# Performance work log

Hardware: AMD Instinct MI355X
Metric: run time of the kernel (lower is better)

## Reference

```python
import math
import jax, jax.numpy as jnp
import numpy as np

T, B, E, H = 1024, 4, 1024, 16
DH = E // H
NUM_BUCKETS = 32
MAX_DISTANCE = 128


def setup_inputs() -> dict:
    key = jax.random.key(0)
    ks = jax.random.split(key, 12)
    s = 0.02
    return {
        "query": jax.random.normal(ks[0], (T, B, E), dtype=jnp.float32),
        "q_w": jax.random.normal(ks[1], (E, E), dtype=jnp.float32) * s,
        "q_b": jax.random.normal(ks[2], (E,), dtype=jnp.float32) * s,
        "k_w": jax.random.normal(ks[3], (E, E), dtype=jnp.float32) * s,
        "k_b": jax.random.normal(ks[4], (E,), dtype=jnp.float32) * s,
        "v_w": jax.random.normal(ks[5], (E, E), dtype=jnp.float32) * s,
        "v_b": jax.random.normal(ks[6], (E,), dtype=jnp.float32) * s,
        "out_w": jax.random.normal(ks[7], (E, E), dtype=jnp.float32) * s,
        "out_b": jnp.zeros((E,), dtype=jnp.float32),
        "rel_bias": jax.random.normal(ks[8], (NUM_BUCKETS, H), dtype=jnp.float32) * s,
        "grep_w": jax.random.normal(ks[9], (8, DH), dtype=jnp.float32) * s,
        "grep_b": jax.random.normal(ks[10], (8,), dtype=jnp.float32) * s,
        "grep_a": jnp.ones((1, H, 1, 1), dtype=jnp.float32),
    }


def _relative_position_buckets(qlen, klen):
    # bidirectional T5-style bucketing
    ctx = jnp.arange(qlen, dtype=jnp.int32)[:, None]
    mem = jnp.arange(klen, dtype=jnp.int32)[None, :]
    rp = mem - ctx  # [qlen, klen]
    n = NUM_BUCKETS // 2
    buckets = (rp > 0).astype(jnp.int32) * n
    arp = jnp.abs(rp)
    max_exact = n // 2
    is_small = arp < max_exact
    # guard log(0): values at arp<max_exact are never selected from the large branch
    large = max_exact + (
        jnp.log(jnp.maximum(arp, 1).astype(jnp.float32) / max_exact)
        / math.log(MAX_DISTANCE / max_exact)
        * (n - max_exact)
    ).astype(jnp.int32)
    large = jnp.minimum(large, n - 1)
    return buckets + jnp.where(is_small, arp, large)


def reference(query, q_w, q_b, k_w, k_b, v_w, v_b, out_w, out_b, rel_bias, grep_w, grep_b, grep_a):
    tgt_len, bsz, embed_dim = query.shape
    scaling = DH ** -0.5

    # relative-position bias [H, T, T]
    buckets = _relative_position_buckets(tgt_len, tgt_len)
    pos_bias = rel_bias[buckets]                     # [T, T, H]
    pos_bias = jnp.transpose(pos_bias, (2, 0, 1))    # [H, T, T]

    # GRU-style gate computed from the *unprojected* query, per head
    qh_raw = jnp.transpose(query, (1, 0, 2)).reshape(bsz, tgt_len, H, DH)
    qh_raw = jnp.transpose(qh_raw, (0, 2, 1, 3))     # [B, H, T, DH]
    g = jnp.einsum("bhtd,ed->bhte", qh_raw, grep_w) + grep_b  # [B,H,T,8]
    g = jax.nn.sigmoid(g.reshape(bsz, H, tgt_len, 2, 4).sum(-1))  # [B,H,T,2]
    gate_a, gate_b = g[..., 0:1], g[..., 1:2]        # [B,H,T,1]
    gate_a_1 = gate_a * (gate_b * grep_a - 1.0) + 2.0
    attn_bias = gate_a_1 * pos_bias[None]            # [B, H, T, T]

    # QKV projections (self-attention: k,v from query)
    q = (query @ q_w.T + q_b) * scaling
    k = query @ k_w.T + k_b
    v = query @ v_w.T + v_b
    qh = jnp.transpose(q.reshape(tgt_len, bsz, H, DH), (1, 2, 0, 3))  # [B,H,T,DH]
    kh = jnp.transpose(k.reshape(tgt_len, bsz, H, DH), (1, 2, 0, 3))
    vh = jnp.transpose(v.reshape(tgt_len, bsz, H, DH), (1, 2, 0, 3))

    scores = jnp.einsum("bhtd,bhsd->bhts", qh, kh) + attn_bias
    probs = jax.nn.softmax(scores, axis=-1)
    ctx = jnp.einsum("bhts,bhsd->bhtd", probs, vh)   # [B,H,T,DH]
    ctx = jnp.transpose(ctx, (2, 0, 1, 3)).reshape(tgt_len, bsz, embed_dim)
    out = ctx @ out_w.T + out_b                      # [T, B, E]
    return out
```

## Files before the change

kernel.cpp:

```cpp
#include <hip/hip_runtime.h>
#include <math.h>

#define T_ 1024
#define B_ 4
#define E_ 1024
#define H_ 16
#define DH_ 64

#define LOG2E 1.44269504088896f

typedef __attribute__((ext_vector_type(8))) __bf16 bf16x8;
typedef __attribute__((ext_vector_type(4))) __bf16 bf16x4;
typedef __attribute__((ext_vector_type(4))) float f32x4;

__device__ __forceinline__ __bf16 f2bf(float x){
  union { unsigned short u; __bf16 b; } cv;
  unsigned u32 = __float_as_uint(x);
  cv.u = (unsigned short)((u32 + 0x7fffu + ((u32 >> 16) & 1u)) >> 16);
  return cv.b;
}
__device__ __forceinline__ __bf16 f2bf_fast(float x){
  union { unsigned short u; __bf16 b; } cv;
  cv.u = (unsigned short)((__float_as_uint(x) + 0x8000u) >> 16);
  return cv.b;
}

__device__ __forceinline__ void glds16(const void* g, void* l){
  __builtin_amdgcn_global_load_lds(
      (__attribute__((address_space(1))) void*)(void*)g,
      (__attribute__((address_space(3))) void*)l,
      16, 0, 0);
}

__global__ __launch_bounds__(256) void prep_kernel(
    const float* __restrict__ q_w, const float* __restrict__ k_w,
    const float* __restrict__ v_w, const float* __restrict__ out_w,
    __bf16* __restrict__ wq, __bf16* __restrict__ wk,
    __bf16* __restrict__ wv, __bf16* __restrict__ wo,
    const float* __restrict__ query, const float* __restrict__ gw,
    const float* __restrict__ gb, const float* __restrict__ ga,
    float* __restrict__ gates, __bf16* __restrict__ qbf,
    const float* __restrict__ rel_bias, float* __restrict__ tab)
{
  const int bid = blockIdx.x;
  const int tid = threadIdx.x;
  if (bid < 4096){
    const float* a; __bf16* o;
    switch (bid >> 10){
      case 0: a = q_w;  o = wq; break;
      case 1: a = k_w;  o = wk; break;
      case 2: a = v_w;  o = wv; break;
      default: a = out_w; o = wo; break;
    }
    int i = ((bid & 1023) * 256 + tid) * 4;
    float4 v = *(const float4*)(a + i);
    bf16x4 r;
    r[0] = f2bf(v.x); r[1] = f2bf(v.y); r[2] = f2bf(v.z); r[3] = f2bf(v.w);
    *(bf16x4*)(o + i) = r;
  } else if (bid < 4352){
    int t = (bid - 4096) * 4 + (tid >> 6);
    int bh = tid & 63;
    int h = bh & 15;
    const float* q = query + (size_t)t * E_ * B_ + bh * 64;
    __bf16* qo = qbf + (size_t)t * E_ * B_ + bh * 64;
    float g[8];
    #pragma unroll
    for (int e = 0; e < 8; e++) g[e] = gb[e];
    #pragma unroll
    for (int c = 0; c < 8; c++){
      float4 v0 = *(const float4*)(q + c * 8);
      float4 v1 = *(const float4*)(q + c * 8 + 4);
      bf16x8 o;
      o[0] = f2bf(v0.x); o[1] = f2bf(v0.y); o[2] = f2bf(v0.z); o[3] = f2bf(v0.w);
      o[4] = f2bf(v1.x); o[5] = f2bf(v1.y); o[6] = f2bf(v1.z); o[7] = f2bf(v1.w);
      *(bf16x8*)(qo + c * 8) = o;
      #pragma unroll
      for (int e = 0; e < 8; e++){
        const float* w = gw + e * 64 + c * 8;
        g[e] += v0.x * w[0] + v0.y * w[1] + v0.z * w[2] + v0.w * w[3]
              + v1.x * w[4] + v1.y * w[5] + v1.z * w[6] + v1.w * w[7];
      }
    }
    float a0 = (g[0] + g[1]) + (g[2] + g[3]);
    float a1 = (g[4] + g[5]) + (g[6] + g[7]);
    float sa = 1.f / (1.f + __expf(-a0));
    float sb = 1.f / (1.f + __expf(-a1));
    gates[bh * T_ + t] = (sa * (sb * ga[h] - 1.0f) + 2.0f) * LOG2E;
  } else {
    int tb = bid - 4352;
    int h = tb >> 3;
    int i = (tb & 7) * 256 + tid;
    if (i < 2047){
      int rp = i - 1023;
      int base = rp > 0 ? 16 : 0;
      int arp = rp < 0 ? -rp : rp;
      int off;
      if (arp < 8) off = arp;
      else {
        float val = (logf((float)arp * 0.125f) / 2.772588722239781f) * 8.0f;
        int lg = (int)val;
        off = 8 + (lg > 7 ? 7 : lg);
      }
      tab[h * 2047 + i] = rel_bias[(base + off) * H_ + h];
    }
  }
}

__global__ __launch_bounds__(256, 2) void gemm_qkv(
    const __bf16* __restrict__ A,
    const __bf16* __restrict__ W0, const __bf16* __restrict__ W1, const __bf16* __restrict__ W2,
    const float* __restrict__ b0, const float* __restrict__ b1, const float* __restrict__ b2,
    __bf16* out0, __bf16* out1, __bf16* out2)
{
  __shared__ __bf16 As[128 * 64];
  __shared__ __bf16 Bs[3][64 * 64];
  const int tid = threadIdx.x;
  const int lane = tid & 63, wid = tid >> 6;
  const int l15 = lane & 15, quad = lane >> 4;
  const int dd = blockIdx.x;
  const int j = dd >> 3;
  const int m0 = ((dd & 7) * 4 + (j & 3)) * 128;
  const int nt = j >> 2;
  const int n0 = nt * 64;

  f32x4 acc[3][2][4];
  #pragma unroll
  for (int z = 0; z < 3; z++)
    #pragma unroll
    for (int i = 0; i < 2; i++)
      #pragma unroll
      for (int jj = 0; jj < 4; jj++){
        acc[z][i][jj][0] = 0.f; acc[z][i][jj][1] = 0.f;
        acc[z][i][jj][2] = 0.f; acc[z][i][jj][3] = 0.f;
      }

  const int grow = lane >> 3;
  const int gcol = (((lane & 7) ^ grow) * 8);
  const int sw = (l15 & 7);

  for (int k0 = 0; k0 < E_; k0 += 64){
    __syncthreads();
    #pragma unroll
    for (int r = 0; r < 4; r++){
      int rb = wid * 32 + r * 8;
      glds16(A + (size_t)(m0 + rb + grow) * E_ + k0 + gcol, &As[rb * 64]);
    }
    #pragma unroll
    for (int r = 0; r < 2; r++){
      int rb = wid * 16 + r * 8;
      glds16(W0 + (size_t)(n0 + rb + grow) * E_ + k0 + gcol, &Bs[0][rb * 64]);
      glds16(W1 + (size_t)(n0 + rb + grow) * E_ + k0 + gcol, &Bs[1][rb * 64]);
      glds16(W2 + (size_t)(n0 + rb + grow) * E_ + k0 + gcol, &Bs[2][rb * 64]);
    }
    __syncthreads();
    #pragma unroll
    for (int kq = 0; kq < 2; kq++){
      const int ce = ((kq * 4 + quad) ^ sw) * 8;
      bf16x8 am[2];
      #pragma unroll
      for (int i = 0; i < 2; i++) am[i] = *(const bf16x8*)&As[(wid * 32 + i * 16 + l15) * 64 + ce];
      #pragma unroll
      for (int z = 0; z < 3; z++){
        bf16x8 bn[4];
        #pragma unroll
        for (int jj = 0; jj < 4; jj++) bn[jj] = *(const bf16x8*)&Bs[z][(jj * 16 + l15) * 64 + ce];
        #pragma unroll
        for (int i = 0; i < 2; i++)
          #pragma unroll
          for (int jj = 0; jj < 4; jj++)
            acc[z][i][jj] = __builtin_amdgcn_mfma_f32_16x16x32_bf16(am[i], bn[jj], acc[z][i][jj], 0, 0, 0);
      }
    }
  }

  #pragma unroll
  for (int z = 0; z < 2; z++){
    __bf16* outp = z ? out1 : out0;
    const float* bias = z ? b1 : b0;
    const float scale = z ? 1.0f : 0.125f * LOG2E;
    #pragma unroll
    for (int i = 0; i < 2; i++){
      const int row0 = m0 + wid * 32 + i * 16 + quad * 4;
      #pragma unroll
      for (int jj = 0; jj < 4; jj++){
        const int col = n0 + jj * 16 + l15;
        const float bc = bias[col];
        const int d2 = col & 63;
        #pragma unroll
        for (int r = 0; r < 4; r++){
          float v = (acc[z][i][jj][r] + bc) * scale;
          int row = row0 + r;
          int t = row >> 2, bb = row & 3;
          outp[(size_t)((bb * H_ + nt) * T_ + t) * DH_ + d2] = f2bf(v);
        }
      }
    }
  }

  __syncthreads();
  __bf16 (*vbuf)[4][32] = (__bf16 (*)[4][32])&As[0];
  #pragma unroll
  for (int i = 0; i < 2; i++){
    const int t_local = wid * 8 + i * 4 + quad;
    #pragma unroll
    for (int jj = 0; jj < 4; jj++){
      const int nl = jj * 16 + l15;
      const float bc = b2[n0 + nl];
      #pragma unroll
      for (int r = 0; r < 4; r++)
        vbuf[nl][r][t_local] = f2bf(acc[2][i][jj][r] + bc);
    }
  }
  __syncthreads();
  {
    const int nl = tid >> 2;
    const int bb = tid & 3;
    __bf16* dst = out2 + (size_t)((bb * H_ + nt) * DH_ + nl) * T_ + (m0 >> 2);
    const __bf16* src = &vbuf[nl][bb][0];
    #pragma unroll
    for (int c = 0; c < 4; c++)
      *(bf16x8*)(dst + c * 8) = *(const bf16x8*)(src + c * 8);
  }
}

__global__ __launch_bounds__(256) void gemm_out(
    const __bf16* __restrict__ A, const __bf16* __restrict__ W,
    const float* __restrict__ bias, float* __restrict__ out)
{
  __shared__ __bf16 As[64 * 64];
  __shared__ __bf16 Bs[128 * 64];
  const int tid = threadIdx.x;
  const int lane = tid & 63, wid = tid >> 6;
  const int l15 = lane & 15, quad = lane >> 4;
  const int wm = wid >> 1, wn = wid & 1;
  const int dd = blockIdx.x;
  const int j = dd >> 3;
  const int m0 = ((dd & 7) * 8 + (j & 7)) * 64;
  const int n0 = (j >> 3) * 128;

  f32x4 acc[2][4];
  #pragma unroll
  for (int i = 0; i < 2; i++)
    #pragma unroll
    for (int jj = 0; jj < 4; jj++){
      acc[i][jj][0] = 0.f; acc[i][jj][1] = 0.f; acc[i][jj][2] = 0.f; acc[i][jj][3] = 0.f;
    }

  const int grow = lane >> 3;
  const int gcol = (((lane & 7) ^ grow) * 8);
  const int sw = (l15 & 7);

  for (int k0 = 0; k0 < E_; k0 += 64){
    __syncthreads();
    #pragma unroll
    for (int r = 0; r < 2; r++){
      int rbA = wid * 16 + r * 8;
      glds16(A + (size_t)(m0 + rbA + grow) * E_ + k0 + gcol, &As[rbA * 64]);
    }
    #pragma unroll
    for (int r = 0; r < 4; r++){
      int rbB = wid * 32 + r * 8;
      glds16(W + (size_t)(n0 + rbB + grow) * E_ + k0 + gcol, &Bs[rbB * 64]);
    }
    __syncthreads();
    #pragma unroll
    for (int kq = 0; kq < 2; kq++){
      const int ce = ((kq * 4 + quad) ^ sw) * 8;
      bf16x8 am[2], bn[4];
      #pragma unroll
      for (int i = 0; i < 2; i++) am[i] = *(const bf16x8*)&As[(wm * 32 + i * 16 + l15) * 64 + ce];
      #pragma unroll
      for (int jj = 0; jj < 4; jj++) bn[jj] = *(const bf16x8*)&Bs[(wn * 64 + jj * 16 + l15) * 64 + ce];
      #pragma unroll
      for (int i = 0; i < 2; i++)
        #pragma unroll
        for (int jj = 0; jj < 4; jj++)
          acc[i][jj] = __builtin_amdgcn_mfma_f32_16x16x32_bf16(am[i], bn[jj], acc[i][jj], 0, 0, 0);
    }
  }

  #pragma unroll
  for (int i = 0; i < 2; i++){
    const int row0 = m0 + wm * 32 + i * 16 + quad * 4;
    #pragma unroll
    for (int jj = 0; jj < 4; jj++){
      const int col = n0 + wn * 64 + jj * 16 + l15;
      const float bc = bias[col];
      #pragma unroll
      for (int r = 0; r < 4; r++)
        out[(size_t)(row0 + r) * E_ + col] = acc[i][jj][r] + bc;
    }
  }
}

__global__ __launch_bounds__(256) void attn_kernel(
    const __bf16* __restrict__ qg, const __bf16* __restrict__ kg, const __bf16* __restrict__ vgT,
    const float* __restrict__ gates, const float* __restrict__ tab,
    __bf16* __restrict__ ctx)
{
  const int LDP = 72;
  __shared__ __bf16 Ks[2][64 * 64];
  __shared__ __bf16 Vt[2][64 * 64];
  __shared__ __bf16 Pt[4][2][16 * LDP];
  __shared__ float tabh[2048];

  const int tid = threadIdx.x;
  const int lane = tid & 63, wid = tid >> 6;
  const int l15 = lane & 15, quad = lane >> 4;
  const int dgrid = blockIdx.x;
  const int j = dgrid >> 3;
  const int bh = (dgrid & 7) + 8 * (j & 7);
  const int tq = j >> 3;
  const int b = bh >> 4, h = bh & 15;
  const __bf16* qb = qg + (size_t)bh * T_ * DH_;
  const __bf16* kb = kg + (size_t)bh * T_ * DH_;
  const __bf16* vb = vgT + (size_t)bh * DH_ * T_;

  for (int i = tid; i < 2047; i += 256) tabh[i] = tab[h * 2047 + i];

  const int t0w = tq * 128 + wid * 32;
  bf16x8 bq[2][2];
  float g[2];
  int ibase[2];
  #pragma unroll
  for (int tg = 0; tg < 2; tg++){
    int t_lane = t0w + tg * 16 + l15;
    bq[tg][0] = *(const bf16x8*)(qb + (size_t)t_lane * DH_ + quad * 8);
    bq[tg][1] = *(const bf16x8*)(qb + (size_t)t_lane * DH_ + 32 + quad * 8);
    g[tg] = gates[bh * T_ + t_lane];
    ibase[tg] = 1023 - t_lane;
  }

  const int grow = lane >> 3;
  const int gcol = (((lane & 7) ^ grow) * 8);
  const int swf = (l15 & 7);

  float l_run[2] = {0.f, 0.f};
  f32x4 O[2][4];
  #pragma unroll
  for (int tg = 0; tg < 2; tg++)
    #pragma unroll
    for (int mt = 0; mt < 4; mt++){ O[tg][mt][0]=0.f; O[tg][mt][1]=0.f; O[tg][mt][2]=0.f; O[tg][mt][3]=0.f; }

  #pragma unroll
  for (int r = 0; r < 2; r++){
    int rb = wid * 16 + r * 8;
    glds16(kb + (size_t)(rb + grow) * DH_ + gcol, &Ks[0][rb * 64]);
    glds16(vb + (size_t)(rb + grow) * T_ + gcol, &Vt[0][rb * 64]);
  }
  __syncthreads();

  for (int it = 0; it < 16; it++){
    const int s0 = it * 64;
    const int cur = it & 1;

    if (it < 15){
      const int sn = s0 + 64;
      #pragma unroll
      for (int r = 0; r < 2; r++){
        int rb = wid * 16 + r * 8;
        glds16(kb + (size_t)(sn + rb + grow) * DH_ + gcol, &Ks[cur ^ 1][rb * 64]);
        glds16(vb + (size_t)(rb + grow) * T_ + sn + gcol, &Vt[cur ^ 1][rb * 64]);
      }
    }

    f32x4 S[2][4];
    #pragma unroll
    for (int nt = 0; nt < 4; nt++){
      const int rowb = (nt * 16 + l15) * 64;
      bf16x8 ak0 = *(const bf16x8*)&Ks[cur][rowb + ((quad ^ swf) * 8)];
      bf16x8 ak1 = *(const bf16x8*)&Ks[cur][rowb + (((4 + quad) ^ swf) * 8)];
      #pragma unroll
      for (int tg = 0; tg < 2; tg++){
        f32x4 a; a[0]=0.f; a[1]=0.f; a[2]=0.f; a[3]=0.f;
        a = __builtin_amdgcn_mfma_f32_16x16x32_bf16(ak0, bq[tg][0], a, 0, 0, 0);
        a = __builtin_amdgcn_mfma_f32_16x16x32_bf16(ak1, bq[tg][1], a, 0, 0, 0);
        S[tg][nt] = a;
      }
    }

    const int drel = s0 - t0w;
    if (drel >= 160 || drel <= -192){
      const float sv = (drel > 0) ? tabh[1151] : tabh[895];
      #pragma unroll
      for (int tg = 0; tg < 2; tg++){
        const float cb = g[tg] * sv;
        #pragma unroll
        for (int nt = 0; nt < 4; nt++)
          #pragma unroll
          for (int r = 0; r < 4; r++)
            S[tg][nt][r] = __builtin_amdgcn_exp2f(S[tg][nt][r] + cb);
      }
    } else {
      #pragma unroll
      for (int tg = 0; tg < 2; tg++){
        const int ib = ibase[tg] + s0;
        #pragma unroll
        for (int nt = 0; nt < 4; nt++)
          #pragma unroll
          for (int r = 0; r < 4; r++)
            S[tg][nt][r] = __builtin_amdgcn_exp2f(S[tg][nt][r] + g[tg] * tabh[ib + nt * 16 + quad * 4 + r]);
      }
    }

    #pragma unroll
    for (int tg = 0; tg < 2; tg++){
      __bf16* pw = &Pt[wid][tg][0];
      #pragma unroll
      for (int nt = 0; nt < 4; nt++){
        bf16x4 p;
        p[0] = f2bf_fast(S[tg][nt][0]); p[1] = f2bf_fast(S[tg][nt][1]);
        p[2] = f2bf_fast(S[tg][nt][2]); p[3] = f2bf_fast(S[tg][nt][3]);
        *(bf16x4*)&pw[l15 * LDP + nt * 16 + quad * 4] = p;
      }
      float rs = 0.f;
      #pragma unroll
      for (int nt = 0; nt < 4; nt++) rs += (S[tg][nt][0] + S[tg][nt][1]) + (S[tg][nt][2] + S[tg][nt][3]);
      rs += __shfl_xor(rs, 16, 64);
      rs += __shfl_xor(rs, 32, 64);
      l_run[tg] += rs;
    }

    #pragma unroll
    for (int ks = 0; ks < 2; ks++){
      bf16x8 bp[2];
      #pragma unroll
      for (int tg = 0; tg < 2; tg++)
        bp[tg] = *(const bf16x8*)&Pt[wid][tg][l15 * LDP + ks * 32 + quad * 8];
      #pragma unroll
      for (int mt = 0; mt < 4; mt++){
        const int rowb = (mt * 16 + l15) * 64;
        bf16x8 av = *(const bf16x8*)&Vt[cur][rowb + (((ks * 4 + quad) ^ swf) * 8)];
        #pragma unroll
        for (int tg = 0; tg < 2; tg++)
          O[tg][mt] = __builtin_amdgcn_mfma_f32_16x16x32_bf16(av, bp[tg], O[tg][mt], 0, 0, 0);
      }
    }

    __syncthreads();
  }

  #pragma unroll
  for (int tg = 0; tg < 2; tg++){
    const int t_lane = t0w + tg * 16 + l15;
    const float inv = 1.f / l_run[tg];
    #pragma unroll
    for (int mt = 0; mt < 4; mt++){
      bf16x4 o;
      o[0] = f2bf(O[tg][mt][0] * inv); o[1] = f2bf(O[tg][mt][1] * inv);
      o[2] = f2bf(O[tg][mt][2] * inv); o[3] = f2bf(O[tg][mt][3] * inv);
      *(bf16x4*)&ctx[(size_t)(t_lane * B_ + b) * E_ + h * DH_ + mt * 16 + quad * 4] = o;
    }
  }
}

extern "C" void kernel_launch(void* const* d_in, const int* in_sizes, int n_in,
                              void* d_out, int out_size, void* d_ws, size_t ws_size,
                              hipStream_t stream)
{
  (void)in_sizes; (void)n_in; (void)out_size; (void)ws_size;
  const float* query    = (const float*)d_in[0];
  const float* q_w      = (const float*)d_in[1];
  const float* q_b      = (const float*)d_in[2];
  const float* k_w      = (const float*)d_in[3];
  const float* k_b      = (const float*)d_in[4];
  const float* v_w      = (const float*)d_in[5];
  const float* v_b      = (const float*)d_in[6];
  const float* out_w    = (const float*)d_in[7];
  const float* out_b    = (const float*)d_in[8];
  const float* rel_bias = (const float*)d_in[9];
  const float* grep_w   = (const float*)d_in[10];
  const float* grep_b   = (const float*)d_in[11];
  const float* grep_a   = (const float*)d_in[12];

  char* ws = (char*)d_ws;
  size_t off = 0;
  __bf16* qbf = (__bf16*)(ws + off); off += (size_t)4096 * 1024 * 2;
  __bf16* wq  = (__bf16*)(ws + off); off += (size_t)1024 * 1024 * 2;
  __bf16* wk  = (__bf16*)(ws + off); off += (size_t)1024 * 1024 * 2;
  __bf16* wv  = (__bf16*)(ws + off); off += (size_t)1024 * 1024 * 2;
  __bf16* wo  = (__bf16*)(ws + off); off += (size_t)1024 * 1024 * 2;
  __bf16* qh  = (__bf16*)(ws + off); off += (size_t)4096 * 1024 * 2;
  __bf16* kh  = (__bf16*)(ws + off); off += (size_t)4096 * 1024 * 2;
  __bf16* vhT = (__bf16*)(ws + off); off += (size_t)4096 * 1024 * 2;
  __bf16* ctx = (__bf16*)(ws + off); off += (size_t)4096 * 1024 * 2;
  float* gates = (float*)(ws + off); off += (size_t)65536 * 4;
  float* tab   = (float*)(ws + off); off += (size_t)16 * 2047 * 4;

  prep_kernel<<<4480, 256, 0, stream>>>(q_w, k_w, v_w, out_w, wq, wk, wv, wo,
                                        query, grep_w, grep_b, grep_a, gates, qbf,
                                        rel_bias, tab);
  gemm_qkv<<<512, 256, 0, stream>>>(qbf, wq, wk, wv, q_b, k_b, v_b, qh, kh, vhT);
  attn_kernel<<<512, 256, 0, stream>>>(qh, kh, vhT, gates, tab, ctx);
  gemm_out<<<512, 256, 0, stream>>>(ctx, wo, out_b, (float*)d_out);
}
```

Measured before the change: 197.7 us.

## Double-buffer shared-memory tiles in QKV and output projection GEMMs

Both projection GEMMs now keep two LDS buffers and issue the async global-to-LDS loads for the next K tile before running MFMAs on the current one. This removes one barrier per K step and is meant to hide global load latency behind compute. The cost is double the LDS per block (the QKV kernel grows to about 80KB), which may lower occupancy below the launch-bounds target. Correctness depends on glds16 completion being covered by __syncthreads.

```diff
diff --git a/kernel.cpp b/kernel.cpp
--- a/kernel.cpp
+++ b/kernel.cpp
@@ -112,8 +112,8 @@
     const float* __restrict__ b0, const float* __restrict__ b1, const float* __restrict__ b2,
     __bf16* out0, __bf16* out1, __bf16* out2)
 {
-  __shared__ __bf16 As[128 * 64];
-  __shared__ __bf16 Bs[3][64 * 64];
+  __shared__ __bf16 As[2][128 * 64];
+  __shared__ __bf16 Bs[2][3][64 * 64];
   const int tid = threadIdx.x;
   const int lane = tid & 63, wid = tid >> 6;
   const int l15 = lane & 15, quad = lane >> 4;
@@ -138,32 +138,33 @@
   const int gcol = (((lane & 7) ^ grow) * 8);
   const int sw = (l15 & 7);
 
-  for (int k0 = 0; k0 < E_; k0 += 64){
-    __syncthreads();
+  auto STAGE = [&](int bi, int k0){
     #pragma unroll
     for (int r = 0; r < 4; r++){
       int rb = wid * 32 + r * 8;
-      glds16(A + (size_t)(m0 + rb + grow) * E_ + k0 + gcol, &As[rb * 64]);
+      glds16(A + (size_t)(m0 + rb + grow) * E_ + k0 + gcol, &As[bi][rb * 64]);
     }
     #pragma unroll
     for (int r = 0; r < 2; r++){
       int rb = wid * 16 + r * 8;
-      glds16(W0 + (size_t)(n0 + rb + grow) * E_ + k0 + gcol, &Bs[0][rb * 64]);
-      glds16(W1 + (size_t)(n0 + rb + grow) * E_ + k0 + gcol, &Bs[1][rb * 64]);
-      glds16(W2 + (size_t)(n0 + rb + grow) * E_ + k0 + gcol, &Bs[2][rb * 64]);
-    }
-    __syncthreads();
+      glds16(W0 + (size_t)(n0 + rb + grow) * E_ + k0 + gcol, &Bs[bi][0][rb * 64]);
+      glds16(W1 + (size_t)(n0 + rb + grow) * E_ + k0 + gcol, &Bs[bi][1][rb * 64]);
+      glds16(W2 + (size_t)(n0 + rb + grow) * E_ + k0 + gcol, &Bs[bi][2][rb * 64]);
+    }
+  };
+
+  auto COMPUTE = [&](int bi){
     #pragma unroll
     for (int kq = 0; kq < 2; kq++){
       const int ce = ((kq * 4 + quad) ^ sw) * 8;
       bf16x8 am[2];
       #pragma unroll
-      for (int i = 0; i < 2; i++) am[i] = *(const bf16x8*)&As[(wid * 32 + i * 16 + l15) * 64 + ce];
+      for (int i = 0; i < 2; i++) am[i] = *(const bf16x8*)&As[bi][(wid * 32 + i * 16 + l15) * 64 + ce];
       #pragma unroll
       for (int z = 0; z < 3; z++){
         bf16x8 bn[4];
         #pragma unroll
-        for (int jj = 0; jj < 4; jj++) bn[jj] = *(const bf16x8*)&Bs[z][(jj * 16 + l15) * 64 + ce];
+        for (int jj = 0; jj < 4; jj++) bn[jj] = *(const bf16x8*)&Bs[bi][z][(jj * 16 + l15) * 64 + ce];
         #pragma unroll
         for (int i = 0; i < 2; i++)
           #pragma unroll
@@ -171,6 +172,17 @@
             acc[z][i][jj] = __builtin_amdgcn_mfma_f32_16x16x32_bf16(am[i], bn[jj], acc[z][i][jj], 0, 0, 0);
       }
     }
+  };
+
+  STAGE(0, 0);
+  __syncthreads();
+  for (int kt = 0; kt < 16; kt += 2){
+    STAGE(1, (kt + 1) * 64);
+    COMPUTE(0);
+    __syncthreads();
+    if (kt + 2 < 16) STAGE(0, (kt + 2) * 64);
+    COMPUTE(1);
+    __syncthreads();
   }
 
   #pragma unroll
@@ -198,7 +210,7 @@
   }
 
   __syncthreads();
-  __bf16 (*vbuf)[4][32] = (__bf16 (*)[4][32])&As[0];
+  __bf16 (*vbuf)[4][32] = (__bf16 (*)[4][32])&As[0][0];
   #pragma unroll
   for (int i = 0; i < 2; i++){
     const int t_local = wid * 8 + i * 4 + quad;
@@ -227,8 +239,8 @@
     const __bf16* __restrict__ A, const __bf16* __restrict__ W,
     const float* __restrict__ bias, float* __restrict__ out)
 {
-  __shared__ __bf16 As[64 * 64];
-  __shared__ __bf16 Bs[128 * 64];
+  __shared__ __bf16 As[2][64 * 64];
+  __shared__ __bf16 Bs[2][128 * 64];
   const int tid = threadIdx.x;
   const int lane = tid & 63, wid = tid >> 6;
   const int l15 = lane & 15, quad = lane >> 4;
@@ -250,33 +262,45 @@
   const int gcol = (((lane & 7) ^ grow) * 8);
   const int sw = (l15 & 7);
 
-  for (int k0 = 0; k0 < E_; k0 += 64){
-    __syncthreads();
+  auto STAGE = [&](int bi, int k0){
     #pragma unroll
     for (int r = 0; r < 2; r++){
       int rbA = wid * 16 + r * 8;
-      glds16(A + (size_t)(m0 + rbA + grow) * E_ + k0 + gcol, &As[rbA * 64]);
+      glds16(A + (size_t)(m0 + rbA + grow) * E_ + k0 + gcol, &As[bi][rbA * 64]);
     }
     #pragma unroll
     for (int r = 0; r < 4; r++){
       int rbB = wid * 32 + r * 8;
-      glds16(W + (size_t)(n0 + rbB + grow) * E_ + k0 + gcol, &Bs[rbB * 64]);
-    }
-    __syncthreads();
+      glds16(W + (size_t)(n0 + rbB + grow) * E_ + k0 + gcol, &Bs[bi][rbB * 64]);
+    }
+  };
+
+  auto COMPUTE = [&](int bi){
     #pragma unroll
     for (int kq = 0; kq < 2; kq++){
       const int ce = ((kq * 4 + quad) ^ sw) * 8;
       bf16x8 am[2], bn[4];
       #pragma unroll
-      for (int i = 0; i < 2; i++) am[i] = *(const bf16x8*)&As[(wm * 32 + i * 16 + l15) * 64 + ce];
-      #pragma unroll
-      for (int jj = 0; jj < 4; jj++) bn[jj] = *(const bf16x8*)&Bs[(wn * 64 + jj * 16 + l15) * 64 + ce];
+      for (int i = 0; i < 2; i++) am[i] = *(const bf16x8*)&As[bi][(wm * 32 + i * 16 + l15) * 64 + ce];
+      #pragma unroll
+      for (int jj = 0; jj < 4; jj++) bn[jj] = *(const bf16x8*)&Bs[bi][(wn * 64 + jj * 16 + l15) * 64 + ce];
       #pragma unroll
       for (int i = 0; i < 2; i++)
         #pragma unroll
         for (int jj = 0; jj < 4; jj++)
           acc[i][jj] = __builtin_amdgcn_mfma_f32_16x16x32_bf16(am[i], bn[jj], acc[i][jj], 0, 0, 0);
     }
+  };
+
+  STAGE(0, 0);
+  __syncthreads();
+  for (int kt = 0; kt < 16; kt += 2){
+    STAGE(1, (kt + 1) * 64);
+    COMPUTE(0);
+    __syncthreads();
+    if (kt + 2 < 16) STAGE(0, (kt + 2) * 64);
+    COMPUTE(1);
+    __syncthreads();
   }
 
   #pragma unroll
```

New measurement: 203.4 us. 2.9% more time.

## Retile QKV GEMM to 256x256 blocks with double-buffered interleaved prefetch

Applied to the files above, without the earlier changes.

The fused QKV projection GEMM now uses 512-thread blocks computing 256x256 output tiles, with each block covering a single one of the Q/K/V weight matrices, so the grid shrinks from 512 to 192 blocks. A double-buffered LDS pipeline issues the next K-slice's global-to-LDS loads in chunks between MFMA phases, separated by raw barriers and with raised wave priority around the MFMA bursts. The aim is higher arithmetic intensity per LDS byte and hiding global-load latency behind compute. The cost is 128KB of LDS per block and 192 blocks on a 256-CU part, which may leave many CUs idle.

```diff
diff --git a/kernel.cpp b/kernel.cpp
--- a/kernel.cpp
+++ b/kernel.cpp
@@ -31,6 +31,9 @@
       (__attribute__((address_space(3))) void*)l,
       16, 0, 0);
 }
+
+#define PBAR() do { asm volatile("" ::: "memory"); __builtin_amdgcn_s_barrier(); asm volatile("" ::: "memory"); } while(0)
+#define VDRAIN() asm volatile("s_waitcnt vmcnt(0)" ::: "memory")
 
 __global__ __launch_bounds__(256) void prep_kernel(
     const float* __restrict__ q_w, const float* __restrict__ k_w,
@@ -106,120 +109,151 @@
   }
 }
 
-__global__ __launch_bounds__(256, 2) void gemm_qkv(
+__global__ __launch_bounds__(512, 2) void gemm_qkv(
     const __bf16* __restrict__ A,
     const __bf16* __restrict__ W0, const __bf16* __restrict__ W1, const __bf16* __restrict__ W2,
     const float* __restrict__ b0, const float* __restrict__ b1, const float* __restrict__ b2,
     __bf16* out0, __bf16* out1, __bf16* out2)
 {
-  __shared__ __bf16 As[128 * 64];
-  __shared__ __bf16 Bs[3][64 * 64];
+  __shared__ __bf16 smem[65536];
   const int tid = threadIdx.x;
   const int lane = tid & 63, wid = tid >> 6;
   const int l15 = lane & 15, quad = lane >> 4;
+  const int wr = wid >> 2, wc = wid & 3;
   const int dd = blockIdx.x;
   const int j = dd >> 3;
-  const int m0 = ((dd & 7) * 4 + (j & 3)) * 128;
-  const int nt = j >> 2;
-  const int n0 = nt * 64;
-
-  f32x4 acc[3][2][4];
-  #pragma unroll
-  for (int z = 0; z < 3; z++)
-    #pragma unroll
-    for (int i = 0; i < 2; i++)
-      #pragma unroll
-      for (int jj = 0; jj < 4; jj++){
-        acc[z][i][jj][0] = 0.f; acc[z][i][jj][1] = 0.f;
-        acc[z][i][jj][2] = 0.f; acc[z][i][jj][3] = 0.f;
-      }
+  const int bm = (dd & 7) * 2 + (j & 1);
+  const int bnb = j >> 1;
+  const int m0 = bm * 256;
+  const int n0 = bnb * 256;
+  const int z  = n0 >> 10;
+  const int nz = n0 & 1023;
+  const __bf16* Wp = (z == 0 ? W0 : (z == 1 ? W1 : W2)) + (size_t)nz * E_;
 
   const int grow = lane >> 3;
   const int gcol = (((lane & 7) ^ grow) * 8);
   const int sw = (l15 & 7);
 
-  for (int k0 = 0; k0 < E_; k0 += 64){
-    __syncthreads();
-    #pragma unroll
-    for (int r = 0; r < 4; r++){
-      int rb = wid * 32 + r * 8;
-      glds16(A + (size_t)(m0 + rb + grow) * E_ + k0 + gcol, &As[rb * 64]);
-    }
-    #pragma unroll
-    for (int r = 0; r < 2; r++){
-      int rb = wid * 16 + r * 8;
-      glds16(W0 + (size_t)(n0 + rb + grow) * E_ + k0 + gcol, &Bs[0][rb * 64]);
-      glds16(W1 + (size_t)(n0 + rb + grow) * E_ + k0 + gcol, &Bs[1][rb * 64]);
-      glds16(W2 + (size_t)(n0 + rb + grow) * E_ + k0 + gcol, &Bs[2][rb * 64]);
-    }
-    __syncthreads();
-    #pragma unroll
-    for (int kq = 0; kq < 2; kq++){
-      const int ce = ((kq * 4 + quad) ^ sw) * 8;
-      bf16x8 am[2];
-      #pragma unroll
-      for (int i = 0; i < 2; i++) am[i] = *(const bf16x8*)&As[(wid * 32 + i * 16 + l15) * 64 + ce];
-      #pragma unroll
-      for (int z = 0; z < 3; z++){
-        bf16x8 bn[4];
-        #pragma unroll
-        for (int jj = 0; jj < 4; jj++) bn[jj] = *(const bf16x8*)&Bs[z][(jj * 16 + l15) * 64 + ce];
-        #pragma unroll
-        for (int i = 0; i < 2; i++)
-          #pragma unroll
-          for (int jj = 0; jj < 4; jj++)
-            acc[z][i][jj] = __builtin_amdgcn_mfma_f32_16x16x32_bf16(am[i], bn[jj], acc[z][i][jj], 0, 0, 0);
-      }
-    }
-  }
-
-  #pragma unroll
-  for (int z = 0; z < 2; z++){
+  f32x4 acc[8][4];
+  #pragma unroll
+  for (int i = 0; i < 8; i++)
+    #pragma unroll
+    for (int jj = 0; jj < 4; jj++){
+      acc[i][jj][0] = 0.f; acc[i][jj][1] = 0.f; acc[i][jj][2] = 0.f; acc[i][jj][3] = 0.f;
+    }
+
+  auto SA = [&](int nb, int kn, int r){
+    const int rb = wid * 32 + r * 8;
+    glds16(A + (size_t)(m0 + rb + grow) * E_ + kn + gcol, smem + nb * 16384 + rb * 64);
+  };
+  auto SB = [&](int nb, int kn, int r){
+    const int rb = wid * 32 + r * 8;
+    glds16(Wp + (size_t)(rb + grow) * E_ + kn + gcol, smem + 32768 + nb * 16384 + rb * 64);
+  };
+
+  bf16x8 am[4], bnr[4];
+  auto RDA = [&](const __bf16* Ac, int mh, int kq){
+    const int ce = ((kq * 4 + quad) ^ sw) * 8;
+    #pragma unroll
+    for (int i = 0; i < 4; i++)
+      am[i] = *(const bf16x8*)&Ac[(wr * 128 + mh * 64 + i * 16 + l15) * 64 + ce];
+  };
+  auto RDB = [&](const __bf16* Bc, int kq){
+    const int ce = ((kq * 4 + quad) ^ sw) * 8;
+    #pragma unroll
+    for (int jj = 0; jj < 4; jj++)
+      bnr[jj] = *(const bf16x8*)&Bc[(wc * 64 + jj * 16 + l15) * 64 + ce];
+  };
+  auto MM = [&](int mh){
+    __builtin_amdgcn_s_setprio(1);
+    #pragma unroll
+    for (int i = 0; i < 4; i++)
+      #pragma unroll
+      for (int jj = 0; jj < 4; jj++)
+        acc[mh * 4 + i][jj] = __builtin_amdgcn_mfma_f32_16x16x32_bf16(am[i], bnr[jj], acc[mh * 4 + i][jj], 0, 0, 0);
+    __builtin_amdgcn_s_setprio(0);
+  };
+
+  #pragma unroll
+  for (int r = 0; r < 4; r++){ SA(0, 0, r); SB(0, 0, r); }
+  VDRAIN();
+  PBAR();
+
+  for (int t = 0; t < 16; t++){
+    const int cb_ = (t & 1) * 16384;
+    const __bf16* Ac = smem + cb_;
+    const __bf16* Bc = smem + 32768 + cb_;
+    const int nb = (t & 1) ^ 1;
+    const int kn = (t + 1) * 64;
+    const bool pf = (t < 15);
+    RDA(Ac, 0, 0); RDB(Bc, 0);
+    if (pf){ SA(nb, kn, 0); SA(nb, kn, 1); }
+    PBAR();
+    MM(0);
+    PBAR();
+    RDA(Ac, 1, 0);
+    if (pf){ SA(nb, kn, 2); SA(nb, kn, 3); }
+    PBAR();
+    MM(1);
+    PBAR();
+    RDA(Ac, 0, 1); RDB(Bc, 1);
+    if (pf){ SB(nb, kn, 0); SB(nb, kn, 1); }
+    PBAR();
+    MM(0);
+    PBAR();
+    RDA(Ac, 1, 1);
+    if (pf){ SB(nb, kn, 2); SB(nb, kn, 3); }
+    PBAR();
+    MM(1);
+    if (pf) VDRAIN();
+    PBAR();
+  }
+
+  if (z < 2){
     __bf16* outp = z ? out1 : out0;
     const float* bias = z ? b1 : b0;
     const float scale = z ? 1.0f : 0.125f * LOG2E;
-    #pragma unroll
-    for (int i = 0; i < 2; i++){
-      const int row0 = m0 + wid * 32 + i * 16 + quad * 4;
-      #pragma unroll
-      for (int jj = 0; jj < 4; jj++){
-        const int col = n0 + jj * 16 + l15;
-        const float bc = bias[col];
-        const int d2 = col & 63;
+    const int nt = (nz >> 6) + wc;
+    #pragma unroll
+    for (int nf = 0; nf < 4; nf++){
+      const int d2 = nf * 16 + l15;
+      const float bc = bias[nt * 64 + d2];
+      #pragma unroll
+      for (int mf = 0; mf < 8; mf++){
+        const int tb = (m0 + wr * 128 + mf * 16 + quad * 4) >> 2;
         #pragma unroll
         for (int r = 0; r < 4; r++){
-          float v = (acc[z][i][jj][r] + bc) * scale;
-          int row = row0 + r;
-          int t = row >> 2, bb = row & 3;
-          outp[(size_t)((bb * H_ + nt) * T_ + t) * DH_ + d2] = f2bf(v);
+          float v = (acc[mf][nf][r] + bc) * scale;
+          outp[(size_t)((r * H_ + nt) * T_ + tb) * DH_ + d2] = f2bf(v);
         }
       }
     }
-  }
-
-  __syncthreads();
-  __bf16 (*vbuf)[4][32] = (__bf16 (*)[4][32])&As[0];
-  #pragma unroll
-  for (int i = 0; i < 2; i++){
-    const int t_local = wid * 8 + i * 4 + quad;
-    #pragma unroll
-    for (int jj = 0; jj < 4; jj++){
-      const int nl = jj * 16 + l15;
-      const float bc = b2[n0 + nl];
-      #pragma unroll
-      for (int r = 0; r < 4; r++)
-        vbuf[nl][r][t_local] = f2bf(acc[2][i][jj][r] + bc);
-    }
-  }
-  __syncthreads();
-  {
-    const int nl = tid >> 2;
-    const int bb = tid & 3;
-    __bf16* dst = out2 + (size_t)((bb * H_ + nt) * DH_ + nl) * T_ + (m0 >> 2);
-    const __bf16* src = &vbuf[nl][bb][0];
-    #pragma unroll
-    for (int c = 0; c < 4; c++)
-      *(bf16x8*)(dst + c * 8) = *(const bf16x8*)(src + c * 8);
+  } else {
+    __bf16 (*vbuf)[4][64] = (__bf16 (*)[4][64])smem;
+    #pragma unroll
+    for (int nf = 0; nf < 4; nf++){
+      const int cbn = wc * 64 + nf * 16 + l15;
+      const float bc = b2[nz + cbn];
+      #pragma unroll
+      for (int mf = 0; mf < 8; mf++){
+        const int tl = wr * 32 + mf * 4 + quad;
+        #pragma unroll
+        for (int r = 0; r < 4; r++)
+          vbuf[cbn][r][tl] = f2bf(acc[mf][nf][r] + bc);
+      }
+    }
+    PBAR();
+    #pragma unroll
+    for (int s = 0; s < 2; s++){
+      const int job = s * 512 + tid;
+      const int vc = job >> 2, bb = job & 3;
+      const int nt = (nz >> 6) + (vc >> 6), d = vc & 63;
+      __bf16* dst = out2 + (size_t)((bb * H_ + nt) * DH_ + d) * T_ + (m0 >> 2);
+      const __bf16* src = &vbuf[vc][bb][0];
+      #pragma unroll
+      for (int c = 0; c < 8; c++)
+        *(bf16x8*)(dst + c * 8) = *(const bf16x8*)(src + c * 8);
+    }
   }
 }
 
@@ -490,7 +524,7 @@
   prep_kernel<<<4480, 256, 0, stream>>>(q_w, k_w, v_w, out_w, wq, wk, wv, wo,
                                         query, grep_w, grep_b, grep_a, gates, qbf,
                                         rel_bias, tab);
-  gemm_qkv<<<512, 256, 0, stream>>>(qbf, wq, wk, wv, q_b, k_b, v_b, qh, kh, vhT);
+  gemm_qkv<<<192, 512, 0, stream>>>(qbf, wq, wk, wv, q_b, k_b, v_b, qh, kh, vhT);
   attn_kernel<<<512, 256, 0, stream>>>(qh, kh, vhT, gates, tab, ctx);
   gemm_out<<<512, 256, 0, stream>>>(ctx, wo, out_b, (float*)d_out);
 }
```

Result: slower. 215.0 us (+8.7%).
